# Optimization experiments

Hardware: AMD Instinct MI355X
Metric: run time of the kernel (lower is better)

Reference implementation:

```python
import jax, jax.numpy as jnp
import numpy as np

N_QUBITS = 11
N_LAYERS = 5
N3 = 3 * N_QUBITS
DIM = 1 << N_QUBITS
C64 = jnp.complex64

CNOT4 = jnp.array([[1., 0., 0., 0.],
                   [0., 1., 0., 0.],
                   [0., 0., 0., 1.],
                   [0., 0., 1., 0.]], dtype=C64)

def _ry(t):
    c, s = jnp.cos(0.5 * t), jnp.sin(0.5 * t)
    return jnp.stack([jnp.stack([c, -s]), jnp.stack([s, c])]).astype(C64)

def _rz(t):
    e = jnp.exp(-0.5j * t.astype(C64))
    z = jnp.zeros((), C64)
    return jnp.stack([jnp.stack([e, z]), jnp.stack([z, jnp.conj(e)])])

def apply_1q(psi, U, q):
    # psi: [B, 2, ..., 2]; qubit 0 is the most-significant axis (kron order lst[0] x lst[1] x ...)
    psi = jnp.moveaxis(psi, 1 + q, -1)
    if U.ndim == 2:
        psi = psi @ U.T
    else:  # per-batch gate [B, 2, 2]
        psi = jnp.einsum('b...j,bij->b...i', psi, U)
    return jnp.moveaxis(psi, -1, 1 + q)

def apply_cnot(psi, c, t):
    psi = jnp.moveaxis(psi, (1 + c, 1 + t), (-2, -1))
    sh = psi.shape
    psi = (psi.reshape(sh[:-2] + (4,)) @ CNOT4.T).reshape(sh)
    return jnp.moveaxis(psi, (-2, -1), (1 + c, 1 + t))

def yzy_layer(psi, params):
    # per-qubit param triples: Ry(p0) Rz(p1) Ry(p2)
    p = params.reshape(N_QUBITS, 3)
    for q in range(N_QUBITS):
        psi = apply_1q(psi, _ry(p[q, 0]), q)
        psi = apply_1q(psi, _rz(p[q, 1]), q)
        psi = apply_1q(psi, _ry(p[q, 2]), q)
    return psi

def _forward(x, w, dimA):
    B = x.shape[0]
    # |0...0> initial state as a [B, 2]*n tensor
    psi = jnp.zeros((B,) + (2,) * N_QUBITS, C64).at[(slice(None),) + (0,) * N_QUBITS].set(1.0)
    # angle embedding, axis='Y': m = cos(x/2) I - i sin(x/2) Y = real rotation matrix
    half = 0.5 * x[:, 0, :]                     # [B, n]
    c, s = jnp.cos(half), jnp.sin(half)
    for q in range(N_QUBITS):
        U = jnp.stack([jnp.stack([c[:, q], -s[:, q]], -1),
                       jnp.stack([s[:, q], c[:, q]], -1)], -2).astype(C64)  # [B,2,2]
        psi = apply_1q(psi, U, q)
    # variational circuit: (YZYLayer + ring_of_cnot) * n_layers + final YZYLayer
    for layer in range(N_LAYERS):
        psi = yzy_layer(psi, w[layer * N3:(layer + 1) * N3])
        for q in range(N_QUBITS):
            psi = apply_cnot(psi, q, (q + 1) % N_QUBITS)
    psi = yzy_layer(psi, w[N_LAYERS * N3:])
    state = psi.reshape(B, DIM)
    # DM = psi psi^dagger, then partial trace over first dimB (most-significant) qubits
    dm = jnp.einsum('bi,bj->bij', state, jnp.conj(state))   # [B, DIM, DIM]
    dB = 1 << (N_QUBITS - dimA)
    dA = 1 << dimA
    return jnp.einsum('bijik->bjk', dm.reshape(B, dB, dA, dB, dA))

def setup_inputs():
    key = jax.random.key(0)
    k1, k2 = jax.random.split(key)
    x = jax.random.uniform(k1, (16, 1, N_QUBITS), jnp.float32, 0.0, 2 * np.pi)
    w_scale = (2 ** 0.5) * 5 ** (-0.5)  # he_std * w_mul with use_wscale=True, lrmul=1
    w = jax.random.uniform(k2, (N3 * (N_LAYERS + 1),), jnp.float32, 0.0, 2 * np.pi) * w_scale
    return {"x": x, "w": w, "dimA": 5}

def reference(x, w, dimA):
    return _forward(x, w, dimA)
```

## Files before the change

### kernel.cpp

```cpp
#include <hip/hip_runtime.h>

#define NQ 11
#define DIM 2048
#define NLAY 6
#define NGATES (NLAY * NQ)

struct c32 { float re, im; };

__host__ __device__ constexpr int ring_f(int u) {
    int P = u ^ (u >> 1); P ^= P >> 2; P ^= P >> 4; P ^= P >> 8;
    return (P & 0x3FF) | (((P ^ (u >> 10)) & 1) << 10);
}
__host__ __device__ constexpr int ring_inv(int v) {
    int o = 0;
    for (int i = 0; i < 9; i++) o |= (((v >> i) ^ (v >> (i + 1))) & 1) << i;
    o |= (((v >> 0) ^ (v >> 9) ^ (v >> 10)) & 1) << 9;
    o |= (((v >> 0) ^ (v >> 10)) & 1) << 10;
    return o;
}
__host__ __device__ constexpr int ring_pow(int v, int k)     { for (int i = 0; i < k; i++) v = ring_f(v);   return v; }
__host__ __device__ constexpr int ring_inv_pow(int v, int k) { for (int i = 0; i < k; i++) v = ring_inv(v); return v; }
__host__ __device__ constexpr int par11(int x) { x ^= x >> 8; x ^= x >> 4; x ^= x >> 2; x ^= x >> 1; return x & 1; }

__host__ __device__ constexpr int mask_of(int L, int b) { return ring_inv_pow(1 << b, L); }
__host__ __device__ constexpr int row_of(int L, int b) {
    int m = 0;
    for (int j = 0; j < 11; j++) m |= ((ring_pow(1 << j, L) >> b) & 1) << j;
    return m;
}
__host__ __device__ constexpr int cgate_index(int L, int Q) {
    int n = 0;
    for (int l = 0; l <= L; l++)
        for (int q = 0; q < (l < L ? NQ : Q); q++)
            if (mask_of(l, 10 - q) >> 9) n++;
    return n;
}
constexpr bool gf2_checks() {
    for (int u = 0; u < DIM; u++)
        if (ring_inv(ring_f(u)) != u || ring_f(ring_inv(u)) != u) return false;
    for (int l = 0; l < NLAY; l++)
        for (int q = 0; q < NQ; q++) {
            const int b = 10 - q;
            if (mask_of(l, b) == 0) return false;
            if (par11(mask_of(l, b) & row_of(l, b)) != 1) return false;
        }
    return true;
}
static_assert(gf2_checks(), "GF2 ring algebra broken");

struct RP5T { int v[8]; };
__host__ __device__ constexpr RP5T mkRP5() { RP5T t{}; for (int r = 0; r < 8; r++) t.v[r] = ring_pow(r, 5); return t; }
constexpr RP5T RP5 = mkRP5();

__device__ __forceinline__ c32 comb(c32 cA, c32 xx, c32 cB, c32 yy) {
    float re =  cA.re * xx.re;
    re = fmaf(-cA.im, xx.im, re);
    re = fmaf( cB.re, yy.re, re);
    re = fmaf(-cB.im, yy.im, re);
    float im =  cA.re * xx.im;
    im = fmaf( cA.im, xx.re, im);
    im = fmaf( cB.re, yy.im, im);
    im = fmaf( cB.im, yy.re, im);
    return { re, im };
}

template<int L, int Q>
__device__ __forceinline__ void do_gate(c32 (&a)[8], const c32 (&g)[4],
                                        c32* exA, c32* exB, int tid) {
    constexpr int b     = 10 - Q;
    constexpr int M     = mask_of(L, b);
    constexpr int RW    = row_of(L, b);
    constexpr int mr    = M & 7;
    constexpr int mt    = M >> 3;
    constexpr int mlane = mt & 63;
    constexpr int mwav  = mt >> 6;

    const c32 m00 = g[0], m01 = g[1], m10 = g[2], m11 = g[3];
    const int sl = __popc(tid & (RW >> 3)) & 1;
    const c32 cO0 = sl ? m11 : m00, cP0 = sl ? m10 : m01;
    const c32 cO1 = sl ? m00 : m11, cP1 = sl ? m01 : m10;

    if constexpr (mwav != 0) {
        c32* buf = (cgate_index(L, Q) & 1) ? exB : exA;
#pragma unroll
        for (int r = 0; r < 8; r++) buf[(r << 8) | tid] = a[r];
        __syncthreads();
#pragma unroll
        for (int r = 0; r < 8; r++) {
            const c32 pv = buf[((r ^ mr) << 8) | (tid ^ mt)];
            const int cr = __popc(r & (RW & 7)) & 1;
            a[r] = cr ? comb(cO1, a[r], cP1, pv) : comb(cO0, a[r], cP0, pv);
        }
    } else if constexpr (mlane != 0 && mr == 0) {
#pragma unroll
        for (int r = 0; r < 8; r++) {
            const c32 pv { __shfl_xor(a[r].re, mlane, 64), __shfl_xor(a[r].im, mlane, 64) };
            const int cr = __popc(r & (RW & 7)) & 1;
            a[r] = cr ? comb(cO1, a[r], cP1, pv) : comb(cO0, a[r], cP0, pv);
        }
    } else if constexpr (mlane != 0) {
        constexpr int piv = mr & (-mr);
#pragma unroll
        for (int r0 = 0; r0 < 8; r0++) if (!(r0 & piv)) {
            const int r1 = r0 ^ mr;
            const c32 o0 = a[r0], o1 = a[r1];
            const c32 pv0 { __shfl_xor(o1.re, mlane, 64), __shfl_xor(o1.im, mlane, 64) };
            const c32 pv1 { __shfl_xor(o0.re, mlane, 64), __shfl_xor(o0.im, mlane, 64) };
            const int cr0 = __popc(r0 & (RW & 7)) & 1;
            const int cr1 = cr0 ^ (__popc(mr & (RW & 7)) & 1);
            a[r0] = cr0 ? comb(cO1, o0, cP1, pv0) : comb(cO0, o0, cP0, pv0);
            a[r1] = cr1 ? comb(cO1, o1, cP1, pv1) : comb(cO0, o1, cP0, pv1);
        }
    } else {
        constexpr int piv = mr & (-mr);
#pragma unroll
        for (int r0 = 0; r0 < 8; r0++) if (!(r0 & piv)) {
            const int r1 = r0 ^ mr;
            const c32 o0 = a[r0], o1 = a[r1];
            const int cr0 = __popc(r0 & (RW & 7)) & 1;
            a[r0] = cr0 ? comb(cO1, o0, cP1, o1) : comb(cO0, o0, cP0, o1);
            a[r1] = cr0 ? comb(cO0, o1, cP0, o0) : comb(cO1, o1, cP1, o0);
        }
    }
}

template<int L, int Q>
__device__ __forceinline__ void run_gates(c32 (&a)[8], const c32 (*gates)[4],
                                          c32* exA, c32* exB, int tid) {
    do_gate<L, Q>(a, gates[L * NQ + Q], exA, exB, tid);
    if constexpr (Q < NQ - 1)       run_gates<L, Q + 1>(a, gates, exA, exB, tid);
    else if constexpr (L < NLAY - 1) run_gates<L + 1, 0>(a, gates, exA, exB, tid);
}

__global__ __launch_bounds__(256) void qsim_kernel(
    const float* __restrict__ x,
    const float* __restrict__ w,
    float* __restrict__ out)
{
    __shared__ c32 exA[DIM];
    __shared__ c32 exB[DIM];
    __shared__ c32 gates[NGATES][4];

    const int b = blockIdx.x;
    const int tid = threadIdx.x;

    if (tid < NGATES) {
        const int l = tid / NQ, q = tid % NQ;
        const float* p = &w[l * 3 * NQ + q * 3];
        float c0, s0, cz, sz, c2, s2;
        sincosf(0.5f * p[0], &s0, &c0);
        sincosf(0.5f * p[1], &sz, &cz);
        sincosf(0.5f * p[2], &s2, &c2);
        c32 A00 = {  cz * c0, -sz * c0 };
        c32 A01 = { -cz * s0,  sz * s0 };
        c32 A10 = {  cz * s0,  sz * s0 };
        c32 A11 = {  cz * c0,  sz * c0 };
        c32 M00 = { c2 * A00.re - s2 * A10.re, c2 * A00.im - s2 * A10.im };
        c32 M01 = { c2 * A01.re - s2 * A11.re, c2 * A01.im - s2 * A11.im };
        c32 M10 = { s2 * A00.re + c2 * A10.re, s2 * A00.im + c2 * A10.im };
        c32 M11 = { s2 * A01.re + c2 * A11.re, s2 * A01.im + c2 * A11.im };
        if (l == 0) {
            float ce, se;
            sincosf(0.5f * x[b * NQ + q], &se, &ce);
            c32 N00 = { M00.re * ce + M01.re * se, M00.im * ce + M01.im * se };
            c32 N01 = { M01.re * ce - M00.re * se, M01.im * ce - M00.im * se };
            c32 N10 = { M10.re * ce + M11.re * se, M10.im * ce + M11.im * se };
            c32 N11 = { M11.re * ce - M10.re * se, M11.im * ce - M10.im * se };
            M00 = N00; M01 = N01; M10 = N10; M11 = N11;
        }
        gates[tid][0] = M00; gates[tid][1] = M01;
        gates[tid][2] = M10; gates[tid][3] = M11;
    }

    c32 a[8];
#pragma unroll
    for (int r = 0; r < 8; r++) a[r] = { 0.f, 0.f };
    if (tid == 0) a[0].re = 1.f;
    __syncthreads();

    run_gates<0, 0>(a, gates, exA, exB, tid);

    __syncthreads();
    int T = tid << 3;
#pragma unroll
    for (int k = 0; k < 5; k++) T = ring_f(T);
#pragma unroll
    for (int r = 0; r < 8; r++) exA[T ^ RP5.v[r]] = a[r];
    __syncthreads();

    const int j0 = (tid >> 4) << 1, k0 = (tid & 15) << 1;
    float r00re = 0.f, r00im = 0.f, r01re = 0.f, r01im = 0.f;
    float r10re = 0.f, r10im = 0.f, r11re = 0.f, r11im = 0.f;
#pragma unroll 8
    for (int i = 0; i < 64; i++) {
        const c32 A0 = exA[i * 32 + j0], A1 = exA[i * 32 + j0 + 1];
        const c32 B0 = exA[i * 32 + k0], B1 = exA[i * 32 + k0 + 1];
        r00re = fmaf(A0.re, B0.re, fmaf( A0.im, B0.im, r00re));
        r00im = fmaf(A0.im, B0.re, fmaf(-A0.re, B0.im, r00im));
        r01re = fmaf(A0.re, B1.re, fmaf( A0.im, B1.im, r01re));
        r01im = fmaf(A0.im, B1.re, fmaf(-A0.re, B1.im, r01im));
        r10re = fmaf(A1.re, B0.re, fmaf( A1.im, B0.im, r10re));
        r10im = fmaf(A1.im, B0.re, fmaf(-A1.re, B0.im, r10im));
        r11re = fmaf(A1.re, B1.re, fmaf( A1.im, B1.im, r11re));
        r11im = fmaf(A1.im, B1.re, fmaf(-A1.re, B1.im, r11im));
    }
    float* o = out + b * 1024;
    o[ j0      * 32 + k0    ] = r00re;
    o[ j0      * 32 + k0 + 1] = r01re;
    o[(j0 + 1) * 32 + k0    ] = r10re;
    o[(j0 + 1) * 32 + k0 + 1] = r11re;
    o += 16384;
    o[ j0      * 32 + k0    ] = r00im;
    o[ j0      * 32 + k0 + 1] = r01im;
    o[(j0 + 1) * 32 + k0    ] = r10im;
    o[(j0 + 1) * 32 + k0 + 1] = r11im;
}

extern "C" void kernel_launch(void* const* d_in, const int* in_sizes, int n_in,
                              void* d_out, int out_size, void* d_ws, size_t ws_size,
                              hipStream_t stream) {
    const float* x = (const float*)d_in[0];
    const float* w = (const float*)d_in[1];
    float* out = (float*)d_out;
    qsim_kernel<<<16, 256, 0, stream>>>(x, w, out);
}
```

Baseline: 77.78 us.

## Plan GF(2) register layouts per segment to minimize LDS exchanges

Adds a compile-time planner that greedily groups gates into segments whose masks can be made wave-local under a per-segment linear change of basis over GF(2). Each segment boundary becomes a single LDS exchange that both applies the cut gate and remaps the state into the next segment's layout. The intent is to cut the number of block-wide barriers and shared-memory round trips, with the count fixed at six. In exchange, the LDS read addresses become XOR-scattered, which can raise bank conflicts, and the final write-out uses the last segment's basis.

```diff
diff --git a/kernel.cpp b/kernel.cpp
--- a/kernel.cpp
+++ b/kernel.cpp
@@ -27,13 +27,6 @@
     int m = 0;
     for (int j = 0; j < 11; j++) m |= ((ring_pow(1 << j, L) >> b) & 1) << j;
     return m;
-}
-__host__ __device__ constexpr int cgate_index(int L, int Q) {
-    int n = 0;
-    for (int l = 0; l <= L; l++)
-        for (int q = 0; q < (l < L ? NQ : Q); q++)
-            if (mask_of(l, 10 - q) >> 9) n++;
-    return n;
 }
 constexpr bool gf2_checks() {
     for (int u = 0; u < DIM; u++)
@@ -48,9 +41,137 @@
 }
 static_assert(gf2_checks(), "GF2 ring algebra broken");
 
-struct RP5T { int v[8]; };
-__host__ __device__ constexpr RP5T mkRP5() { RP5T t{}; for (int r = 0; r < 8; r++) t.v[r] = ring_pow(r, 5); return t; }
-constexpr RP5T RP5 = mkRP5();
+struct M11 { int col[11]; };
+
+__host__ __device__ constexpr int mapv(const M11& A, int x) {
+    int y = 0;
+    for (int i = 0; i < 11; ++i) if ((x >> i) & 1) y ^= A.col[i];
+    return y;
+}
+__host__ __device__ constexpr M11 inv11(const M11& A) {
+    unsigned rowa[11] = {};
+    for (int r = 0; r < 11; ++r) {
+        unsigned v = 0;
+        for (int c = 0; c < 11; ++c) v |= ((unsigned)(A.col[c] >> r) & 1u) << c;
+        rowa[r] = v | (1u << (11 + r));
+    }
+    for (int c = 0; c < 11; ++c) {
+        int piv = -1;
+        for (int r = c; r < 11; ++r) if ((rowa[r] >> c) & 1u) { piv = r; break; }
+        if (piv < 0) continue;
+        unsigned tmp = rowa[c]; rowa[c] = rowa[piv]; rowa[piv] = tmp;
+        for (int r = 0; r < 11; ++r)
+            if (r != c && ((rowa[r] >> c) & 1u)) rowa[r] ^= rowa[c];
+    }
+    M11 R{};
+    for (int c = 0; c < 11; ++c) {
+        int v = 0;
+        for (int r = 0; r < 11; ++r) v |= (int)((rowa[r] >> (11 + c)) & 1u) << r;
+        R.col[c] = v;
+    }
+    return R;
+}
+__host__ __device__ constexpr int rotv(int t) { return ((t & 7) << 8) | (t >> 3); }
+
+struct Plan {
+    int kind[NGATES];
+    int tmask[NGATES];
+    int trow[NGATES];
+    int gcol[NGATES][11];
+    int dslot[NGATES];
+    int cidx[NGATES];
+    int ucol[11];
+    int ncuts;
+    int ok;
+};
+
+__host__ __device__ constexpr int topbit11(int x) { int b = -1; for (int i = 0; i < 11; ++i) if ((x >> i) & 1) b = i; return b; }
+
+__host__ __device__ constexpr int reduce_ech(int r, const int* ech, int ne) {
+    bool ch = true;
+    while (ch && r) {
+        ch = false;
+        for (int i = 0; i < ne; ++i) {
+            const int tb = topbit11(ech[i]);
+            if (tb >= 0 && ((r >> tb) & 1)) { r ^= ech[i]; ch = true; }
+        }
+    }
+    return r;
+}
+
+__host__ __device__ constexpr Plan mkplan() {
+    Plan P{};
+    P.ok = 1;
+    constexpr int MAXSEG = 16;
+    M11 C[MAXSEG] = {};
+    int nb[MAXSEG] = {};
+    int lastseg = 0;
+    {
+        int ech[11] = {}; int ne = 0; int seg = 0;
+        for (int g = 0; g < NGATES; ++g) {
+            const int m = mask_of(g / 11, 10 - g % 11);
+            const int r = reduce_ech(m, ech, ne);
+            if (r != 0 && ne == 9) {
+                P.kind[g] = 1; P.cidx[g] = P.ncuts++;
+                seg++; ne = 0;
+                if (seg >= MAXSEG) { P.ok = 0; return P; }
+            } else {
+                P.kind[g] = 0;
+                if (r != 0) { ech[ne++] = r; C[seg].col[nb[seg]++] = m; }
+            }
+        }
+        lastseg = seg;
+        for (int s = 0; s <= seg; ++s) {
+            for (int j = 0; j < 11 && nb[s] < 11; ++j) {
+                int e2[11] = {}; int n2 = 0;
+                for (int i = 0; i < nb[s]; ++i) {
+                    const int rr = reduce_ech(C[s].col[i], e2, n2);
+                    if (rr) e2[n2++] = rr;
+                }
+                if (reduce_ech(1 << j, e2, n2) != 0) C[s].col[nb[s]++] = 1 << j;
+            }
+            if (nb[s] != 11) P.ok = 0;
+        }
+    }
+    {
+        M11 IC[MAXSEG] = {};
+        for (int s = 0; s <= lastseg; ++s) {
+            IC[s] = inv11(C[s]);
+            for (int i = 0; i < 11; ++i)
+                if (mapv(IC[s], C[s].col[i]) != (1 << i)) P.ok = 0;
+        }
+        int cur = 0;
+        for (int g = 0; g < NGATES; ++g) {
+            const int L = g / 11, b = 10 - g % 11;
+            const int m = mask_of(L, b), rw = row_of(L, b);
+            if (P.kind[g] == 0) {
+                const int tm = mapv(IC[cur], m);
+                P.tmask[g] = tm;
+                int tr = 0;
+                for (int i = 0; i < 11; ++i) tr |= par11(rw & C[cur].col[i]) << i;
+                P.trow[g] = tr;
+                if ((tm >> 9) != 0 || tm == 0) P.ok = 0;
+                if (par11(tr & tm) != 1) P.ok = 0;
+            } else {
+                const int so = cur, sn = cur + 1;
+                for (int i = 0; i < 11; ++i)
+                    P.gcol[g][i] = rotv(mapv(IC[so], C[sn].col[i]));
+                P.dslot[g] = rotv(mapv(IC[so], m));
+                int tr = 0;
+                for (int i = 0; i < 11; ++i) tr |= par11(rw & C[sn].col[i]) << i;
+                P.trow[g] = tr;
+                cur = sn;
+            }
+        }
+        if (cur != lastseg) P.ok = 0;
+        for (int i = 0; i < 11; ++i) P.ucol[i] = ring_pow(C[cur].col[i], 5);
+    }
+    return P;
+}
+
+constexpr Plan PL = mkplan();
+static_assert(PL.ok == 1, "layout plan construction failed");
+static_assert(PL.ncuts == 6, "expected exactly 6 LDS exchanges");
 
 __device__ __forceinline__ c32 comb(c32 cA, c32 xx, c32 cB, c32 yy) {
     float re =  cA.re * xx.re;
@@ -64,72 +185,98 @@
     return { re, im };
 }
 
-template<int L, int Q>
-__device__ __forceinline__ void do_gate(c32 (&a)[8], const c32 (&g)[4],
-                                        c32* exA, c32* exB, int tid) {
-    constexpr int b     = 10 - Q;
-    constexpr int M     = mask_of(L, b);
-    constexpr int RW    = row_of(L, b);
-    constexpr int mr    = M & 7;
-    constexpr int mt    = M >> 3;
-    constexpr int mlane = mt & 63;
-    constexpr int mwav  = mt >> 6;
-
-    const c32 m00 = g[0], m01 = g[1], m10 = g[2], m11 = g[3];
-    const int sl = __popc(tid & (RW >> 3)) & 1;
+template<int g>
+__device__ __forceinline__ void seg_gate(c32 (&a)[8], const c32 (&gm)[4], int tid) {
+    constexpr int TMv = PL.tmask[g];
+    constexpr int TRv = PL.trow[g];
+    constexpr int mr = TMv & 7;
+    constexpr int mlane = (TMv >> 3) & 63;
+    static_assert((TMv >> 9) == 0 && TMv != 0, "seg gate must be wave-local");
+
+    const c32 m00 = gm[0], m01 = gm[1], m10 = gm[2], m11 = gm[3];
+    const int sl = __popc(tid & (TRv >> 3)) & 1;
     const c32 cO0 = sl ? m11 : m00, cP0 = sl ? m10 : m01;
     const c32 cO1 = sl ? m00 : m11, cP1 = sl ? m01 : m10;
 
-    if constexpr (mwav != 0) {
-        c32* buf = (cgate_index(L, Q) & 1) ? exB : exA;
-#pragma unroll
-        for (int r = 0; r < 8; r++) buf[(r << 8) | tid] = a[r];
-        __syncthreads();
-#pragma unroll
-        for (int r = 0; r < 8; r++) {
-            const c32 pv = buf[((r ^ mr) << 8) | (tid ^ mt)];
-            const int cr = __popc(r & (RW & 7)) & 1;
-            a[r] = cr ? comb(cO1, a[r], cP1, pv) : comb(cO0, a[r], cP0, pv);
-        }
-    } else if constexpr (mlane != 0 && mr == 0) {
-#pragma unroll
-        for (int r = 0; r < 8; r++) {
+    if constexpr (mlane != 0 && mr == 0) {
+#pragma unroll
+        for (int r = 0; r < 8; ++r) {
             const c32 pv { __shfl_xor(a[r].re, mlane, 64), __shfl_xor(a[r].im, mlane, 64) };
-            const int cr = __popc(r & (RW & 7)) & 1;
+            const int cr = __popc(r & (TRv & 7)) & 1;
             a[r] = cr ? comb(cO1, a[r], cP1, pv) : comb(cO0, a[r], cP0, pv);
         }
     } else if constexpr (mlane != 0) {
         constexpr int piv = mr & (-mr);
 #pragma unroll
-        for (int r0 = 0; r0 < 8; r0++) if (!(r0 & piv)) {
+        for (int r0 = 0; r0 < 8; ++r0) if (!(r0 & piv)) {
             const int r1 = r0 ^ mr;
             const c32 o0 = a[r0], o1 = a[r1];
             const c32 pv0 { __shfl_xor(o1.re, mlane, 64), __shfl_xor(o1.im, mlane, 64) };
             const c32 pv1 { __shfl_xor(o0.re, mlane, 64), __shfl_xor(o0.im, mlane, 64) };
-            const int cr0 = __popc(r0 & (RW & 7)) & 1;
-            const int cr1 = cr0 ^ (__popc(mr & (RW & 7)) & 1);
+            const int cr0 = __popc(r0 & (TRv & 7)) & 1;
+            const int cr1 = cr0 ^ (__popc(mr & (TRv & 7)) & 1);
             a[r0] = cr0 ? comb(cO1, o0, cP1, pv0) : comb(cO0, o0, cP0, pv0);
             a[r1] = cr1 ? comb(cO1, o1, cP1, pv1) : comb(cO0, o1, cP0, pv1);
         }
     } else {
         constexpr int piv = mr & (-mr);
 #pragma unroll
-        for (int r0 = 0; r0 < 8; r0++) if (!(r0 & piv)) {
+        for (int r0 = 0; r0 < 8; ++r0) if (!(r0 & piv)) {
             const int r1 = r0 ^ mr;
             const c32 o0 = a[r0], o1 = a[r1];
-            const int cr0 = __popc(r0 & (RW & 7)) & 1;
+            const int cr0 = __popc(r0 & (TRv & 7)) & 1;
             a[r0] = cr0 ? comb(cO1, o0, cP1, o1) : comb(cO0, o0, cP0, o1);
             a[r1] = cr0 ? comb(cO0, o1, cP0, o0) : comb(cO1, o1, cP1, o0);
         }
     }
 }
 
-template<int L, int Q>
-__device__ __forceinline__ void run_gates(c32 (&a)[8], const c32 (*gates)[4],
-                                          c32* exA, c32* exB, int tid) {
-    do_gate<L, Q>(a, gates[L * NQ + Q], exA, exB, tid);
-    if constexpr (Q < NQ - 1)       run_gates<L, Q + 1>(a, gates, exA, exB, tid);
-    else if constexpr (L < NLAY - 1) run_gates<L + 1, 0>(a, gates, exA, exB, tid);
+template<int g>
+__device__ __forceinline__ void cut_gate(c32 (&a)[8], const c32 (&gm)[4],
+                                         c32* exA, c32* exB, int tid) {
+    constexpr int TRv = PL.trow[g];
+    constexpr int DS  = PL.dslot[g];
+    constexpr int CI  = PL.cidx[g];
+    constexpr int G0 = PL.gcol[g][0], G1 = PL.gcol[g][1], G2 = PL.gcol[g][2];
+    constexpr int G3 = PL.gcol[g][3], G4 = PL.gcol[g][4], G5 = PL.gcol[g][5];
+    constexpr int G6 = PL.gcol[g][6], G7 = PL.gcol[g][7], G8 = PL.gcol[g][8];
+    constexpr int G9 = PL.gcol[g][9], G10 = PL.gcol[g][10];
+
+    c32* buf = (CI & 1) ? exB : exA;
+#pragma unroll
+    for (int r = 0; r < 8; ++r) buf[(r << 8) | tid] = a[r];
+    __syncthreads();
+
+    int base = 0;
+    base ^= (-((tid >> 0) & 1)) & G3;
+    base ^= (-((tid >> 1) & 1)) & G4;
+    base ^= (-((tid >> 2) & 1)) & G5;
+    base ^= (-((tid >> 3) & 1)) & G6;
+    base ^= (-((tid >> 4) & 1)) & G7;
+    base ^= (-((tid >> 5) & 1)) & G8;
+    base ^= (-((tid >> 6) & 1)) & G9;
+    base ^= (-((tid >> 7) & 1)) & G10;
+
+    const c32 m00 = gm[0], m01 = gm[1], m10 = gm[2], m11 = gm[3];
+    const int sl = __popc(tid & (TRv >> 3)) & 1;
+    const c32 cO0 = sl ? m11 : m00, cP0 = sl ? m10 : m01;
+    const c32 cO1 = sl ? m00 : m11, cP1 = sl ? m01 : m10;
+#pragma unroll
+    for (int r = 0; r < 8; ++r) {
+        const int so = base ^ (((r & 1) ? G0 : 0) ^ ((r & 2) ? G1 : 0) ^ ((r & 4) ? G2 : 0));
+        const c32 own = buf[so];
+        const c32 par = buf[so ^ DS];
+        const int cr = __popc(r & (TRv & 7)) & 1;
+        a[r] = cr ? comb(cO1, own, cP1, par) : comb(cO0, own, cP0, par);
+    }
+}
+
+template<int g>
+__device__ __forceinline__ void run_all(c32 (&a)[8], const c32 (*gates)[4],
+                                        c32* exA, c32* exB, int tid) {
+    if constexpr (PL.kind[g] == 1) cut_gate<g>(a, gates[g], exA, exB, tid);
+    else                           seg_gate<g>(a, gates[g], tid);
+    if constexpr (g + 1 < NGATES) run_all<g + 1>(a, gates, exA, exB, tid);
 }
 
 __global__ __launch_bounds__(256) void qsim_kernel(
@@ -174,18 +321,31 @@
 
     c32 a[8];
 #pragma unroll
-    for (int r = 0; r < 8; r++) a[r] = { 0.f, 0.f };
+    for (int r = 0; r < 8; ++r) a[r] = { 0.f, 0.f };
     if (tid == 0) a[0].re = 1.f;
     __syncthreads();
 
-    run_gates<0, 0>(a, gates, exA, exB, tid);
-
-    __syncthreads();
-    int T = tid << 3;
-#pragma unroll
-    for (int k = 0; k < 5; k++) T = ring_f(T);
-#pragma unroll
-    for (int r = 0; r < 8; r++) exA[T ^ RP5.v[r]] = a[r];
+    run_all<0>(a, gates, exA, exB, tid);
+
+    constexpr int U0 = PL.ucol[0], U1 = PL.ucol[1], U2 = PL.ucol[2];
+    constexpr int U3 = PL.ucol[3], U4 = PL.ucol[4], U5 = PL.ucol[5];
+    constexpr int U6 = PL.ucol[6], U7 = PL.ucol[7], U8 = PL.ucol[8];
+    constexpr int U9 = PL.ucol[9], U10 = PL.ucol[10];
+    c32* fb = (PL.ncuts & 1) ? exB : exA;
+    int T = 0;
+    T ^= (-((tid >> 0) & 1)) & U3;
+    T ^= (-((tid >> 1) & 1)) & U4;
+    T ^= (-((tid >> 2) & 1)) & U5;
+    T ^= (-((tid >> 3) & 1)) & U6;
+    T ^= (-((tid >> 4) & 1)) & U7;
+    T ^= (-((tid >> 5) & 1)) & U8;
+    T ^= (-((tid >> 6) & 1)) & U9;
+    T ^= (-((tid >> 7) & 1)) & U10;
+#pragma unroll
+    for (int r = 0; r < 8; ++r) {
+        const int off = ((r & 1) ? U0 : 0) ^ ((r & 2) ? U1 : 0) ^ ((r & 4) ? U2 : 0);
+        fb[T ^ off] = a[r];
+    }
     __syncthreads();
 
     const int j0 = (tid >> 4) << 1, k0 = (tid & 15) << 1;
@@ -193,8 +353,8 @@
     float r10re = 0.f, r10im = 0.f, r11re = 0.f, r11im = 0.f;
 #pragma unroll 8
     for (int i = 0; i < 64; i++) {
-        const c32 A0 = exA[i * 32 + j0], A1 = exA[i * 32 + j0 + 1];
-        const c32 B0 = exA[i * 32 + k0], B1 = exA[i * 32 + k0 + 1];
+        const c32 A0 = fb[i * 32 + j0], A1 = fb[i * 32 + j0 + 1];
+        const c32 B0 = fb[i * 32 + k0], B1 = fb[i * 32 + k0 + 1];
         r00re = fmaf(A0.re, B0.re, fmaf( A0.im, B0.im, r00re));
         r00im = fmaf(A0.im, B0.re, fmaf(-A0.re, B0.im, r00im));
         r01re = fmaf(A0.re, B1.re, fmaf( A0.im, B1.im, r01re));
```

Result: faster. 73.40 us (-5.6%).
